# Kernel optimization log

Measured on AMD Instinct MI355X. Metric: run time of the kernel, lower is better.

Reference implementation:

```python
import jax, jax.numpy as jnp
import numpy as np

STRIDES = (8, 16, 32, 64, 128)
SIZES = ((40, 40), (20, 20), (10, 10), (5, 5), (3, 3))
NUM_CLASSES = 80
SCORE_THR = 0.025
NMS_PRE = 1000
IOU_THR = 0.5
IMG = 320.0  # img_shape hardcoded to (320, 320); clamp uses max_shape[1]
B = 4


def setup_inputs() -> dict:
    key = jax.random.key(0)
    ks = jax.random.split(key, 15)
    inp = {}
    for i, (h, w) in enumerate(SIZES):
        inp[f"cls{i}"] = jax.random.normal(ks[3 * i], (B, NUM_CLASSES, h, w), dtype=jnp.float32)
        # bbox preds are ltrb distances; scale uniform noise to plausible pixel distances
        inp[f"bbox{i}"] = jax.random.uniform(ks[3 * i + 1], (B, 4, h, w), dtype=jnp.float32) * 64.0
        inp[f"ctr{i}"] = jax.random.normal(ks[3 * i + 2], (B, 1, h, w), dtype=jnp.float32)
    return inp


def _priors(h, w, stride):
    # MlvlPointGenerator: (arange + 0.5) * stride, x fastest-varying
    sx = (jnp.arange(w, dtype=jnp.float32) + 0.5) * stride
    sy = (jnp.arange(h, dtype=jnp.float32) + 0.5) * stride
    return jnp.stack([jnp.tile(sx, h), jnp.repeat(sy, w)], axis=-1)  # [h*w, 2]


def _distance2bbox(points, dist):
    x1 = points[:, 0] - dist[:, 0]
    y1 = points[:, 1] - dist[:, 1]
    x2 = points[:, 0] + dist[:, 2]
    y2 = points[:, 1] + dist[:, 3]
    # torch.clamp_ on the whole tensor: min=0, max=max_shape[1]=320
    return jnp.clip(jnp.stack([x1, y1, x2, y2], axis=-1), 0.0, IMG)


def _pairwise_iou(boxes):
    # torchvision-style IoU on [K,4] boxes
    area = (boxes[:, 2] - boxes[:, 0]) * (boxes[:, 3] - boxes[:, 1])
    lt = jnp.maximum(boxes[:, None, :2], boxes[None, :, :2])
    rb = jnp.minimum(boxes[:, None, 2:], boxes[None, :, 2:])
    wh = jnp.maximum(rb - lt, 0.0)
    inter = wh[..., 0] * wh[..., 1]
    union = area[:, None] + area[None, :] - inter
    safe = jnp.where(union > 0.0, union, 1.0)
    return jnp.where(union > 0.0, inter / safe, 0.0)


def _single(cls_l, bbox_l, ctr_l):
    """Post-process one image. Returns fixed-size (dets [K,5], labels [K], keep [K] bool)."""
    scores_l, labels_l, boxes_l, valid_l = [], [], [], []
    for lvl in range(5):
        h, w = SIZES[lvl]
        pri = _priors(h, w, STRIDES[lvl])
        s = jax.nn.sigmoid(jnp.transpose(cls_l[lvl], (1, 2, 0)).reshape(-1, NUM_CLASSES)).reshape(-1)
        bp = jnp.transpose(bbox_l[lvl], (1, 2, 0)).reshape(-1, 4)
        sf = jax.nn.sigmoid(jnp.transpose(ctr_l[lvl], (1, 2, 0)).reshape(-1))
        # filter_scores_and_topk: mask scores <= thr to -1 so they sort last; fixed-size top_k
        k = min(NMS_PRE, s.shape[0])
        top_s, top_i = jax.lax.top_k(jnp.where(s > SCORE_THR, s, -1.0), k)
        anchor = top_i // NUM_CLASSES
        label = top_i % NUM_CLASSES
        valid = top_s > SCORE_THR
        boxes = _distance2bbox(pri[anchor], bp[anchor])
        # scores multiplied by centerness score factor (FCOS)
        scores_l.append(jnp.where(valid, top_s * sf[anchor], -1.0))
        labels_l.append(label)
        boxes_l.append(boxes)
        valid_l.append(valid)
    scores = jnp.concatenate(scores_l)          # [K]
    labels = jnp.concatenate(labels_l)          # [K]
    boxes = jnp.concatenate(boxes_l, axis=0)    # [K,4]
    valid = jnp.concatenate(valid_l)            # [K]
    # sort by final score descending (NMS processes in score order)
    order = jnp.argsort(-scores)
    scores = scores[order]
    labels = labels[order]
    boxes = boxes[order]
    valid = valid[order]
    # batched_nms: per-class coordinate offset trick
    max_coord = boxes.max()
    off = boxes + (labels.astype(jnp.float32) * (max_coord + 1.0))[:, None]
    iou = _pairwise_iou(off)  # [K,K]
    K = scores.shape[0]
    idx = jnp.arange(K)

    def body(i, keep):
        sup = (iou[i] > IOU_THR) & (idx > i) & keep[i]
        return keep & jnp.logical_not(sup)

    keep = jax.lax.fori_loop(0, K, body, valid)
    dets = jnp.concatenate([boxes, scores[:, None]], axis=-1)  # [K,5]
    return dets, labels, keep


def reference(cls0, cls1, cls2, cls3, cls4, bbox0, bbox1, bbox2, bbox3, bbox4, ctr0, ctr1, ctr2, ctr3, ctr4):
    cls_l = (cls0, cls1, cls2, cls3, cls4)
    bbox_l = (bbox0, bbox1, bbox2, bbox3, bbox4)
    ctr_l = (ctr0, ctr1, ctr2, ctr3, ctr4)
    return jax.vmap(_single)(cls_l, bbox_l, ctr_l)
```

## Files before the change

### kernel.cpp

```cpp
#include <hip/hip_runtime.h>
#include <stdint.h>


#define BN 4
#define NC 80
#define TOT 170720
#define KTOT 4720
#define NWIN 74
#define NJT 19
#define TIE_CAP 4096
#define IMGSZ 320.0f
#define PAIR_CAP 131072
#define LDSP 12288

struct InPtrs {
  const float* cls[5];
  const float* bbox[5];
  const float* ctr[5];
};

__device__ __forceinline__ uint32_t f2s(float f) {
  uint32_t x = __float_as_uint(f);
  return (x & 0x80000000u) ? ~x : (x | 0x80000000u);
}
__device__ __forceinline__ float s2f(uint32_t s) {
  uint32_t x = (s & 0x80000000u) ? (s & 0x7fffffffu) : ~s;
  return __uint_as_float(x);
}
__device__ __forceinline__ float sigmoid32(float v) {
  float e = (float)exp(-(double)v);
  return __fdiv_rn(1.0f, __fadd_rn(1.0f, e));
}
__device__ __forceinline__ void lvl_of(int e, int& l, int& le) {
  if (e < 128000)      { l = 0; le = e; }
  else if (e < 160000) { l = 1; le = e - 128000; }
  else if (e < 168000) { l = 2; le = e - 160000; }
  else if (e < 170000) { l = 3; le = e - 168000; }
  else                 { l = 4; le = e - 170000; }
}
__device__ __forceinline__ int kl_of(int l) {
  constexpr int KL[5] = {1000, 1000, 1000, 1000, 720};
  return KL[l];
}
__device__ __forceinline__ float clip32(float v) {
  return fminf(fmaxf(v, 0.0f), IMGSZ);
}
__device__ __forceinline__ void tile_of(int t, int& l, int& p0) {
  if (t < 25)       { l = 0; p0 = t * 64; }
  else if (t < 32)  { l = 1; p0 = (t - 25) * 64; }
  else if (t < 34)  { l = 2; p0 = (t - 32) * 64; }
  else if (t == 34) { l = 3; p0 = 0; }
  else              { l = 4; p0 = 0; }
}
__device__ __forceinline__ int iou_gt(float bx1, float by1, float bx2, float by2,
                                      float bai, float4 o) {
  float ta_ = __fmul_rn(__fsub_rn(o.z, o.x), __fsub_rn(o.w, o.y));
  float ltx = fmaxf(bx1, o.x), lty = fmaxf(by1, o.y);
  float rbx = fminf(bx2, o.z), rby = fminf(by2, o.w);
  float wd = fmaxf(__fsub_rn(rbx, ltx), 0.0f);
  float hg = fmaxf(__fsub_rn(rby, lty), 0.0f);
  float inter = __fmul_rn(wd, hg);
  float asum = __fadd_rn(bai, ta_);
  float uni  = __fsub_rn(asum, inter);
  float iou  = (uni > 0.0f) ? __fdiv_rn(inter, uni) : 0.0f;
  return (iou > 0.5f) ? 1 : 0;
}

__global__ void k_score(InPtrs in, uint32_t* __restrict__ su, uint32_t* __restrict__ hist0) {
  int b = blockIdx.y;
  int tl, p0; tile_of(blockIdx.x, tl, p0);
  constexpr int HWc[5]  = {1600, 400, 100, 25, 9};
  constexpr int LOFF[5] = {0, 128000, 160000, 168000, 170000};
  int hw = HWc[tl];
  int tw = min(64, hw - p0);
  int tid = threadIdx.x;
  __shared__ uint32_t lu[64 * 81];
  __shared__ uint32_t lh[1024];
  for (int i = tid; i < 1024; i += 256) lh[i] = 0;
  __syncthreads();
  int pf = tid & 63;
  if (pf < tw) {
    const float* cp = in.cls[tl] + (size_t)b * NC * hw + p0 + pf;
    for (int c = tid >> 6; c < NC; c += 4) {
      float v = cp[(size_t)c * hw];
      float s = sigmoid32(v);
      float m = (s > 0.025f) ? s : -1.0f;
      uint32_t u = f2s(m);
      lu[pf * 81 + c] = u;
      atomicAdd(&lh[u >> 22], 1u);
    }
  }
  __syncthreads();
  int bl = b * 5 + tl;
  for (int i = tid; i < 1024; i += 256)
    if (lh[i]) atomicAdd(&hist0[(size_t)bl * 1024 + i], lh[i]);
  int n = tw * NC;
  uint32_t* dst = su + (size_t)b * TOT + LOFF[tl] + p0 * NC;
  for (int idx = tid; idx < n; idx += 256)
    dst[idx] = lu[(idx / 80) * 81 + (idx % 80)];
}

__global__ void k_scan1(const uint32_t* __restrict__ su, const uint32_t* __restrict__ mpfx,
                        uint32_t* __restrict__ hist1) {
  int b = blockIdx.y;
  int tid = threadIdx.x;
  int e0 = blockIdx.x * 256;
  int e = e0 + tid;
  int l0, le0; lvl_of(e0, l0, le0);
  __shared__ uint32_t lh[2][1024];
  for (int i = tid; i < 2048; i += 256) lh[i >> 10][i & 1023] = 0;
  __syncthreads();
  if (e < TOT) {
    int l, le; lvl_of(e, l, le);
    uint32_t C = mpfx[b * 5 + l];
    uint32_t u = su[(size_t)b * TOT + e];
    if ((u >> 22) == (C >> 22)) atomicAdd(&lh[l - l0][(u >> 12) & 1023u], 1u);
  }
  __syncthreads();
  for (int s = 0; s < 2; s++) {
    int l = l0 + s;
    if (l >= 5) break;
    int bl = b * 5 + l;
    for (int i = tid; i < 1024; i += 256)
      if (lh[s][i]) atomicAdd(&hist1[(size_t)bl * 1024 + i], lh[s][i]);
  }
}

__global__ void k_scan2(const uint32_t* __restrict__ su, const uint32_t* __restrict__ mpfx,
                        uint32_t* __restrict__ hist2) {
  int b = blockIdx.y;
  int e = blockIdx.x * blockDim.x + threadIdx.x;
  if (e >= TOT) return;
  int l, le; lvl_of(e, l, le);
  int bl = b * 5 + l;
  uint32_t C = mpfx[bl];
  uint32_t u = su[(size_t)b * TOT + e];
  if ((u >> 12) == (C >> 12))
    atomicAdd(&hist2[(size_t)bl * 4096 + (u & 4095u)], 1u);
}

__global__ void k_findp(const uint32_t* __restrict__ hist, uint32_t* __restrict__ mpfx,
                        uint32_t* __restrict__ mk, int nbins, int shift, int pass) {
  int bl = blockIdx.x;
  uint32_t k = (pass == 0) ? (uint32_t)kl_of(bl % 5) : mk[bl];
  const uint32_t* h = hist + (size_t)bl * nbins;
  __shared__ uint32_t gsum[256];
  int tid = threadIdx.x;
  int per = nbins / 256;
  int base = tid * per;
  uint32_t s = 0;
  for (int i = 0; i < per; i++) s += h[base + i];
  gsum[tid] = s;
  __syncthreads();
  uint32_t above = 0;
  for (int t = tid + 1; t < 256; t++) above += gsum[t];
  if (above < k && above + s >= k) {
    uint32_t cum = above;
    for (int bin = base + per - 1; bin >= base; bin--) {
      uint32_t c = h[bin];
      if (cum < k && cum + c >= k) {
        uint32_t pfx = (pass == 0) ? 0u : mpfx[bl];
        mpfx[bl] = pfx | ((uint32_t)bin << shift);
        mk[bl] = k - cum;
        break;
      }
      cum += c;
    }
  }
}

__global__ void k_compact(const uint32_t* __restrict__ su, const uint32_t* __restrict__ mpfx,
                          uint32_t* __restrict__ selcnt, uint32_t* __restrict__ tiecnt,
                          uint32_t* __restrict__ selu, uint32_t* __restrict__ seli,
                          uint32_t* __restrict__ tiei) {
  int b = blockIdx.y;
  int tid = threadIdx.x;
  int e0 = blockIdx.x * 256;
  int e = e0 + tid;
  int l0, le0; lvl_of(e0, l0, le0);
  __shared__ uint32_t cnt[2], tcnt[2], gbase[2], tgbase[2];
  __shared__ uint32_t su_s[2][256], si_s[2][256];
  __shared__ uint32_t ti_s[2][256];
  if (tid < 2) { cnt[tid] = 0u; tcnt[tid] = 0u; }
  __syncthreads();
  if (e < TOT) {
    int l, le; lvl_of(e, l, le);
    int slot = l - l0;
    int bl = b * 5 + l;
    uint32_t u = su[(size_t)b * TOT + e];
    uint32_t C = mpfx[bl];
    if (u > C) {
      uint32_t p = atomicAdd(&cnt[slot], 1u);
      su_s[slot][p] = u;
      si_s[slot][p] = (uint32_t)le;
    } else if (u == C) {
      uint32_t p = atomicAdd(&tcnt[slot], 1u);
      ti_s[slot][p] = (uint32_t)le;
    }
  }
  __syncthreads();
  if (tid < 2) {
    int bl = b * 5 + l0 + tid;
    if (cnt[tid])  gbase[tid]  = atomicAdd(&selcnt[bl], cnt[tid]);
    if (tcnt[tid]) tgbase[tid] = atomicAdd(&tiecnt[bl], tcnt[tid]);
  }
  __syncthreads();
  for (int s = 0; s < 2; s++) {
    int bl = b * 5 + l0 + s;
    uint32_t n = cnt[s];
    for (uint32_t t = tid; t < n; t += 256) {
      uint32_t pos = gbase[s] + t;
      selu[(size_t)bl * 1024 + pos] = su_s[s][t];
      seli[(size_t)bl * 1024 + pos] = si_s[s][t];
    }
    uint32_t tn = tcnt[s];
    for (uint32_t t = tid; t < tn; t += 256) {
      uint32_t pos = tgbase[s] + t;
      if (pos < TIE_CAP) tiei[(size_t)bl * TIE_CAP + pos] = ti_s[s][t];
    }
  }
}

__global__ void k_ties(const uint32_t* __restrict__ mpfx, const uint32_t* __restrict__ mk,
                       const uint32_t* __restrict__ tiecnt, const uint32_t* __restrict__ tiei,
                       uint32_t* __restrict__ selu, uint32_t* __restrict__ seli) {
  int bl = blockIdx.x;
  int l = bl % 5;
  uint32_t C = mpfx[bl];
  uint32_t T = mk[bl];
  uint32_t G = (uint32_t)kl_of(l) - T;
  uint32_t Tc = tiecnt[bl];
  if (Tc > TIE_CAP) Tc = TIE_CAP;
  __shared__ uint32_t sh[TIE_CAP];
  for (uint32_t t = threadIdx.x; t < Tc; t += blockDim.x) sh[t] = tiei[(size_t)bl * TIE_CAP + t];
  __syncthreads();
  for (uint32_t t = threadIdx.x; t < Tc; t += blockDim.x) {
    uint32_t my = sh[t];
    uint32_t rank = 0;
    for (uint32_t q = 0; q < Tc; q++) rank += (sh[q] < my) ? 1u : 0u;
    if (rank < T) {
      selu[(size_t)bl * 1024 + G + rank] = C;
      seli[(size_t)bl * 1024 + G + rank] = my;
    }
  }
}

__global__ void k_emit(InPtrs in, const uint32_t* __restrict__ selu, const uint32_t* __restrict__ seli,
                       float* __restrict__ ccs, uint32_t* __restrict__ ccl,
                       uint32_t* __restrict__ ccv, float* __restrict__ ccb) {
  int bl = blockIdx.x;
  int chunk = blockIdx.y;
  int b = bl / 5, l = bl % 5;
  int k = kl_of(l);
  __shared__ uint64_t z[1024];
  int tid = threadIdx.x;
  for (int t = tid; t < 1024; t += 256) {
    if (t < k) {
      uint32_t u = selu[(size_t)bl * 1024 + t];
      uint32_t idx = seli[(size_t)bl * 1024 + t];
      z[t] = (((uint64_t)u) << 32) | (uint32_t)(~idx);
    } else z[t] = 0ull;
  }
  __syncthreads();
  int tg = chunk * 256 + tid;
  if (tg >= k) return;
  uint64_t zi = z[tg];
  uint32_t u = (uint32_t)(zi >> 32);
  uint32_t idx = ~(uint32_t)zi;
  int rank = 0;
  const uint4* z4 = (const uint4*)z;
  for (int j4 = 0; j4 < 512; j4++) {
    uint4 q = z4[j4];
    uint64_t za = (((uint64_t)q.y) << 32) | q.x;
    uint64_t zb = (((uint64_t)q.w) << 32) | q.z;
    rank += (za > zi) ? 1 : 0;
    rank += (zb > zi) ? 1 : 0;
  }
  constexpr int Wc[5]  = {40, 20, 10, 5, 3};
  constexpr int HWc[5] = {1600, 400, 100, 25, 9};
  constexpr float Sc[5] = {8.f, 16.f, 32.f, 64.f, 128.f};
  constexpr int COFF[5] = {0, 1000, 2000, 3000, 4000};
  int w = Wc[l], hw = HWc[l];
  float ms = s2f(u);
  int valid = (ms > 0.025f) ? 1 : 0;
  int p = (int)idx / NC, c = (int)idx % NC;
  int x = p % w, y = p / w;
  float sf = sigmoid32(in.ctr[l][(size_t)b * hw + p]);
  float score = valid ? __fmul_rn(ms, sf) : -1.0f;
  float px = __fmul_rn(__fadd_rn((float)x, 0.5f), Sc[l]);
  float py = __fmul_rn(__fadd_rn((float)y, 0.5f), Sc[l]);
  size_t bb = (size_t)b * 4 * hw;
  float d0 = in.bbox[l][bb + 0 * hw + p];
  float d1 = in.bbox[l][bb + 1 * hw + p];
  float d2 = in.bbox[l][bb + 2 * hw + p];
  float d3 = in.bbox[l][bb + 3 * hw + p];
  float x1 = clip32(__fsub_rn(px, d0)), y1 = clip32(__fsub_rn(py, d1));
  float x2 = clip32(__fadd_rn(px, d2)), y2 = clip32(__fadd_rn(py, d3));
  int o = b * KTOT + COFF[l] + rank;
  ccs[o] = score;
  ccl[o] = (uint32_t)c;
  ccv[o] = (uint32_t)valid;
  ccb[(size_t)o * 4 + 0] = x1; ccb[(size_t)o * 4 + 1] = y1;
  ccb[(size_t)o * 4 + 2] = x2; ccb[(size_t)o * 4 + 3] = y2;
}

__global__ void k_rank(const float* __restrict__ ccs, uint32_t* __restrict__ rankp) {
  int b = blockIdx.z;
  int jt = blockIdx.y;
  int ib = blockIdx.x;
  int tid = threadIdx.x;
  __shared__ uint32_t jk[256];
  int j0 = jt * 256;
  int jn = min(256, KTOT - j0);
  jk[tid] = (tid < jn) ? f2s(ccs[(size_t)b * KTOT + j0 + tid]) : 0u;
  __syncthreads();
  int e = ib * 256 + tid;
  if (e >= KTOT) return;
  uint32_t ke = f2s(ccs[(size_t)b * KTOT + e]);
  int rank = 0;
  const uint4* k4 = (const uint4*)jk;
#pragma unroll 8
  for (int q = 0; q < 64; q++) {
    uint4 kk = k4[q];
    int j = j0 + q * 4;
    rank += ((kk.x > ke) || (kk.x == ke && (j + 0) < e)) ? 1 : 0;
    rank += ((kk.y > ke) || (kk.y == ke && (j + 1) < e)) ? 1 : 0;
    rank += ((kk.z > ke) || (kk.z == ke && (j + 2) < e)) ? 1 : 0;
    rank += ((kk.w > ke) || (kk.w == ke && (j + 3) < e)) ? 1 : 0;
  }
  rankp[((size_t)b * NJT + jt) * KTOT + e] = (uint32_t)rank;
}

__global__ void k_scatter(const float* __restrict__ ccs, const uint32_t* __restrict__ ccl,
                          const uint32_t* __restrict__ ccv, const float* __restrict__ ccb,
                          const uint32_t* __restrict__ rankp,
                          float* __restrict__ ss, uint32_t* __restrict__ sl,
                          uint32_t* __restrict__ sv, float* __restrict__ sb,
                          uint32_t* __restrict__ maxcb) {
  int b = blockIdx.y;
  __shared__ float red[4];
  int tid = threadIdx.x;
  int e = blockIdx.x * 256 + tid;
  float mx = 0.0f;
  if (e < KTOT) {
    uint32_t rank = 0;
    for (int jt = 0; jt < NJT; jt++)
      rank += rankp[((size_t)b * NJT + jt) * KTOT + e];
    int sidx = b * KTOT + e;
    int d = b * KTOT + (int)rank;
    ss[d] = ccs[sidx];
    sl[d] = ccl[sidx];
    sv[d] = ccv[sidx];
    float b0 = ccb[(size_t)sidx * 4 + 0], b1 = ccb[(size_t)sidx * 4 + 1];
    float b2 = ccb[(size_t)sidx * 4 + 2], b3 = ccb[(size_t)sidx * 4 + 3];
    sb[(size_t)d * 4 + 0] = b0; sb[(size_t)d * 4 + 1] = b1;
    sb[(size_t)d * 4 + 2] = b2; sb[(size_t)d * 4 + 3] = b3;
    mx = fmaxf(fmaxf(b0, b1), fmaxf(b2, b3));
  }
  for (int o = 32; o; o >>= 1) mx = fmaxf(mx, __shfl_xor(mx, o));
  if ((tid & 63) == 0) red[tid >> 6] = mx;
  __syncthreads();
  if (tid == 0)
    atomicMax(&maxcb[b], __float_as_uint(fmaxf(fmaxf(red[0], red[1]), fmaxf(red[2], red[3]))));
}

__global__ void k_bits(const uint32_t* __restrict__ sv, unsigned long long* __restrict__ vbits) {
  int w = blockIdx.x, b = blockIdx.y, lane = threadIdx.x;
  int e = w * 64 + lane;
  int pred = (e < KTOT) ? (sv[(size_t)b * KTOT + e] != 0u) : 0;
  unsigned long long m = __ballot(pred);
  if (lane == 0) vbits[b * NWIN + w] = m;
}

__global__ void k_offset(const float* __restrict__ sb, const uint32_t* __restrict__ sl,
                         const uint32_t* __restrict__ maxcb, float* __restrict__ ob,
                         uint32_t* __restrict__ paircnt) {
  if (blockIdx.x == 0 && threadIdx.x < BN) paircnt[threadIdx.x] = 0u;
  int r = blockIdx.x * blockDim.x + threadIdx.x;
  if (r >= BN * KTOT) return;
  int b = r / KTOT;
  float scale = __fadd_rn(__uint_as_float(maxcb[b]), 1.0f);
  float offv = __fmul_rn((float)sl[r], scale);
  float x1 = __fadd_rn(sb[(size_t)r * 4 + 0], offv);
  float y1 = __fadd_rn(sb[(size_t)r * 4 + 1], offv);
  float x2 = __fadd_rn(sb[(size_t)r * 4 + 2], offv);
  float y2 = __fadd_rn(sb[(size_t)r * 4 + 3], offv);
  ob[(size_t)r * 4 + 0] = x1; ob[(size_t)r * 4 + 1] = y1;
  ob[(size_t)r * 4 + 2] = x2; ob[(size_t)r * 4 + 3] = y2;
}

__global__ void k_class(const uint32_t* __restrict__ sl, uint32_t* __restrict__ clist,
                        uint32_t* __restrict__ ccount) {
  int b = blockIdx.y;
  int c = blockIdx.x;
  int tid = threadIdx.x;
  int lane = tid & 63, wv = tid >> 6;
  __shared__ uint32_t woff[4];
  uint32_t* out = clist + ((size_t)b * NC + c) * KTOT;
  uint32_t base = 0;
  for (int chunk = 0; chunk < KTOT; chunk += 256) {
    int e = chunk + tid;
    int pred = (e < KTOT) && (sl[(size_t)b * KTOT + e] == (uint32_t)c);
    unsigned long long bal = __ballot(pred);
    if (lane == 0) woff[wv] = (uint32_t)__popcll(bal);
    __syncthreads();
    uint32_t myoff = base;
    for (int v = 0; v < wv; v++) myoff += woff[v];
    uint32_t tot = woff[0] + woff[1] + woff[2] + woff[3];
    if (pred) {
      uint32_t pos = myoff + (uint32_t)__popcll(bal & ((1ull << lane) - 1ull));
      out[pos] = (uint32_t)e;
    }
    base += tot;
    __syncthreads();
  }
  if (tid == 0) ccount[b * NC + c] = base;
}

__global__ void k_mask2(const float* __restrict__ ob, const uint32_t* __restrict__ clist,
                        const uint32_t* __restrict__ ccount,
                        uint32_t* __restrict__ pairs, uint32_t* __restrict__ paircnt) {
  int b = blockIdx.y;
  int c = blockIdx.x;
  int m = (int)ccount[b * NC + c];
  if (m < 2) return;
  const uint32_t* cl = clist + ((size_t)b * NC + c) * KTOT;
  const float4* ob4 = (const float4*)ob + (size_t)b * KTOT;
  int tid = threadIdx.x;
  __shared__ float4 tb[256];
  __shared__ uint32_t jidx[256];
  __shared__ uint32_t pcnt[256];
  __shared__ uint32_t sbase;
  uint32_t mycnt = 0;
  for (int jt = 0; jt < m; jt += 256) {
    int jn = min(256, m - jt);
    __syncthreads();
    if (tid < jn) { uint32_t gj = cl[jt + tid]; jidx[tid] = gj; tb[tid] = ob4[gj]; }
    __syncthreads();
    for (int i = tid; i < m; i += 256) {
      uint32_t gi = cl[i];
      float4 v = ob4[gi];
      float bai = __fmul_rn(__fsub_rn(v.z, v.x), __fsub_rn(v.w, v.y));
      for (int jj = 0; jj < jn; jj++)
        if (jidx[jj] > gi && iou_gt(v.x, v.y, v.z, v.w, bai, tb[jj])) mycnt++;
    }
  }
  __syncthreads();
  pcnt[tid] = mycnt;
  __syncthreads();
  uint32_t myoff = 0, total = 0;
  for (int t = 0; t < 256; t++) { uint32_t v = pcnt[t]; if (t < tid) myoff += v; total += v; }
  if (total == 0) return;
  if (tid == 0) sbase = atomicAdd(&paircnt[b], total);
  __syncthreads();
  uint32_t base = sbase;
  uint32_t* gp = pairs + (size_t)b * PAIR_CAP;
  uint32_t k = 0;
  for (int jt = 0; jt < m; jt += 256) {
    int jn = min(256, m - jt);
    __syncthreads();
    if (tid < jn) { uint32_t gj = cl[jt + tid]; jidx[tid] = gj; tb[tid] = ob4[gj]; }
    __syncthreads();
    for (int i = tid; i < m; i += 256) {
      uint32_t gi = cl[i];
      float4 v = ob4[gi];
      float bai = __fmul_rn(__fsub_rn(v.z, v.x), __fsub_rn(v.w, v.y));
      for (int jj = 0; jj < jn; jj++) {
        uint32_t gj = jidx[jj];
        if (gj > gi && iou_gt(v.x, v.y, v.z, v.w, bai, tb[jj])) {
          uint32_t pos = base + myoff + k; k++;
          if (pos < PAIR_CAP) gp[pos] = (gi << 13) | gj;
        }
      }
    }
  }
}

__global__ void k_nms(const float* __restrict__ ob,
                      const unsigned long long* __restrict__ vbits,
                      unsigned long long* __restrict__ keepw,
                      const uint32_t* __restrict__ pairs,
                      const uint32_t* __restrict__ paircnt) {
  int b = blockIdx.x;
  int tid = threadIdx.x;
  int lane = tid & 63;
  int wv = tid >> 6;
  __shared__ unsigned long long tdl[NWIN * 64];
  __shared__ unsigned long long svl[NWIN];
  __shared__ unsigned long long sup[NWIN];
  __shared__ unsigned long long kwsh;
  __shared__ uint32_t plp[LDSP];
  __shared__ uint32_t wstart[NWIN + 1];
  __shared__ uint32_t wtmp[NWIN];
  for (int i = tid; i < NWIN * 64; i += 256) tdl[i] = 0ull;
  if (tid < NWIN) { svl[tid] = vbits[b * NWIN + tid]; sup[tid] = 0ull; wtmp[tid] = 0u; }
  uint32_t npairs = paircnt[b];
  bool useP = (npairs <= (uint32_t)PAIR_CAP);
  bool useL = (npairs <= (uint32_t)LDSP);
  const uint32_t* gpl = pairs + (size_t)b * PAIR_CAP;
  __syncthreads();
  unsigned int* sup32 = (unsigned int*)sup;
  unsigned int* tdl32 = (unsigned int*)tdl;
  if (useP) {
    for (uint32_t t = tid; t < npairs; t += 256) {
      uint32_t p = gpl[t];
      int i = (int)(p >> 13), j = (int)(p & 8191u);
      if ((i >> 6) == (j >> 6)) {
        int r = ((i >> 6) * 64 + (i & 63)) * 2 + ((j & 63) >> 5);
        atomicOr(&tdl32[r], 1u << (j & 31));
      } else {
        atomicAdd(&wtmp[i >> 6], 1u);
      }
    }
    __syncthreads();
    if (tid == 0) {
      uint32_t acc = 0;
      for (int w = 0; w < NWIN; w++) { wstart[w] = acc; acc += wtmp[w]; }
      wstart[NWIN] = acc;
    }
    __syncthreads();
    if (tid < NWIN) wtmp[tid] = 0u;
    __syncthreads();
    if (useL) {
      for (uint32_t t = tid; t < npairs; t += 256) {
        uint32_t p = gpl[t];
        int i = (int)(p >> 13), j = (int)(p & 8191u);
        if ((i >> 6) == (j >> 6)) continue;
        uint32_t w = (uint32_t)(i >> 6);
        uint32_t pos = wstart[w] + atomicAdd(&wtmp[w], 1u);
        plp[pos] = p;
      }
    }
    __syncthreads();
    for (int w = 0; w < NWIN; w++) {
      if (wv == 0) {
        unsigned long long row = tdl[w * 64 + lane];
        unsigned long long m = __ballot(row != 0ull);
        unsigned long long sa = sup[w];
        unsigned long long sval = svl[w];
        unsigned int rlo = (unsigned int)row, rhi = (unsigned int)(row >> 32);
        while (m) {
          int i = __ffsll((long long)m) - 1;
          m &= m - 1;
          if (((sval >> i) & 1ull) && !((sa >> i) & 1ull)) {
            unsigned int lo = (unsigned int)__builtin_amdgcn_readlane((int)rlo, i);
            unsigned int hi = (unsigned int)__builtin_amdgcn_readlane((int)rhi, i);
            sa |= (((unsigned long long)hi) << 32) | (unsigned long long)lo;
          }
        }
        unsigned long long kw = sval & ~sa;
        if (lane == 0) { keepw[b * NWIN + w] = kw; kwsh = kw; }
      }
      __syncthreads();
      unsigned long long kw = kwsh;
      if (useL) {
        for (uint32_t t = wstart[w] + tid; t < wstart[w + 1]; t += 256) {
          uint32_t p = plp[t];
          int i = (int)(p >> 13);
          if (!((kw >> (i & 63)) & 1ull)) continue;
          int j = (int)(p & 8191u);
          atomicOr(&sup32[j >> 5], 1u << (j & 31));
        }
      } else {
        for (uint32_t t = tid; t < npairs; t += 256) {
          uint32_t p = gpl[t];
          int i = (int)(p >> 13);
          if ((i >> 6) != w) continue;
          int j = (int)(p & 8191u);
          if ((j >> 6) == w) continue;
          if (!((kw >> (i & 63)) & 1ull)) continue;
          atomicOr(&sup32[j >> 5], 1u << (j & 31));
        }
      }
      __syncthreads();
    }
  } else {
    const float4* ob4 = (const float4*)ob + (size_t)b * KTOT;
    for (int w = 0; w < NWIN; w++) {
      if (wv == 0) {
        int i = w * 64 + lane;
        unsigned long long row = 0ull;
        if (i < KTOT) {
          float4 v = ob4[i];
          float bai = __fmul_rn(__fsub_rn(v.z, v.x), __fsub_rn(v.w, v.y));
          for (int jj = 0; jj < 64; jj++) {
            int j = w * 64 + jj;
            if (j > i && j < KTOT)
              row |= ((unsigned long long)iou_gt(v.x, v.y, v.z, v.w, bai, ob4[j])) << jj;
          }
        }
        unsigned long long m = __ballot(row != 0ull);
        unsigned long long sa = sup[w];
        unsigned long long sval = svl[w];
        unsigned int rlo = (unsigned int)row, rhi = (unsigned int)(row >> 32);
        while (m) {
          int i2 = __ffsll((long long)m) - 1;
          m &= m - 1;
          if (((sval >> i2) & 1ull) && !((sa >> i2) & 1ull)) {
            unsigned int lo = (unsigned int)__builtin_amdgcn_readlane((int)rlo, i2);
            unsigned int hi = (unsigned int)__builtin_amdgcn_readlane((int)rhi, i2);
            sa |= (((unsigned long long)hi) << 32) | (unsigned long long)lo;
          }
        }
        unsigned long long kw = sval & ~sa;
        if (lane == 0) { keepw[b * NWIN + w] = kw; kwsh = kw; }
      }
      __syncthreads();
      unsigned long long kw = kwsh;
      for (int ii = 0; ii < 64; ii++) {
        if (!((kw >> ii) & 1ull)) continue;
        int i = w * 64 + ii;
        if (i >= KTOT) break;
        float4 v = ob4[i];
        float bai = __fmul_rn(__fsub_rn(v.z, v.x), __fsub_rn(v.w, v.y));
        for (int j = (w + 1) * 64 + tid; j < KTOT; j += 256)
          if (iou_gt(v.x, v.y, v.z, v.w, bai, ob4[j]))
            atomicOr(&sup32[j >> 5], 1u << (j & 31));
      }
      __syncthreads();
    }
  }
}

__global__ void k_out(const float* __restrict__ ss, const uint32_t* __restrict__ sl,
                      const float* __restrict__ sb, const unsigned long long* __restrict__ keepw,
                      float* __restrict__ out) {
  int r = blockIdx.x * blockDim.x + threadIdx.x;
  if (r >= BN * KTOT) return;
  int b = r / KTOT;
  int e = r - b * KTOT;
  unsigned int kp = (unsigned int)((keepw[b * NWIN + (e >> 6)] >> (e & 63)) & 1ull);
  out[(size_t)r * 5 + 0] = sb[(size_t)r * 4 + 0];
  out[(size_t)r * 5 + 1] = sb[(size_t)r * 4 + 1];
  out[(size_t)r * 5 + 2] = sb[(size_t)r * 4 + 2];
  out[(size_t)r * 5 + 3] = sb[(size_t)r * 4 + 3];
  out[(size_t)r * 5 + 4] = ss[r];
  out[(size_t)BN * KTOT * 5 + r] = (float)sl[r];
  out[(size_t)BN * KTOT * 6 + r] = kp ? 1.0f : 0.0f;
}

extern "C" void kernel_launch(void* const* d_in, const int* in_sizes, int n_in,
                              void* d_out, int out_size, void* d_ws, size_t ws_size,
                              hipStream_t stream) {
  InPtrs ip;
  for (int l = 0; l < 5; l++) {
    ip.cls[l]  = (const float*)d_in[3 * l + 0];
    ip.bbox[l] = (const float*)d_in[3 * l + 1];
    ip.ctr[l]  = (const float*)d_in[3 * l + 2];
  }

  size_t off = 0;
  auto alloc = [&](size_t n) {
    char* p = (char*)d_ws + off;
    off = (off + n + 255) & ~(size_t)255;
    return p;
  };
  const size_t SU_BYTES   = (size_t)BN * TOT * 4;
  const size_t HIST_BYTES = (20ull * 1024 + 20ull * 1024 + 20ull * 4096) * 4;
  const size_t EXTRA      = 256;
  char* r0p = (char*)alloc(((SU_BYTES + 255) & ~(size_t)255) + HIST_BYTES + EXTRA);
  uint32_t* su    = (uint32_t*)r0p;
  uint32_t* hist0 = (uint32_t*)(r0p + ((SU_BYTES + 255) & ~(size_t)255));
  uint32_t* hist1 = hist0 + 20ull * 1024;
  uint32_t* hist2 = hist1 + 20ull * 1024;
  uint32_t* selcnt = hist2 + 20ull * 4096;
  uint32_t* tiecnt = selcnt + 20;
  uint32_t* maxcb  = tiecnt + 20;

  uint32_t* mpfx   = (uint32_t*)alloc(20 * 4);
  uint32_t* mk     = (uint32_t*)alloc(20 * 4);
  uint32_t* selu   = (uint32_t*)alloc(20ull * 1024 * 4);
  uint32_t* seli   = (uint32_t*)alloc(20ull * 1024 * 4);
  uint32_t* tiei   = (uint32_t*)alloc(20ull * TIE_CAP * 4);
  float*    ccs    = (float*)   alloc((size_t)BN * KTOT * 4);
  uint32_t* ccl    = (uint32_t*)alloc((size_t)BN * KTOT * 4);
  uint32_t* ccv    = (uint32_t*)alloc((size_t)BN * KTOT * 4);
  float*    ccb    = (float*)   alloc((size_t)BN * KTOT * 16);
  float*    ss     = (float*)   alloc((size_t)BN * KTOT * 4);
  uint32_t* sl     = (uint32_t*)alloc((size_t)BN * KTOT * 4);
  uint32_t* sv     = (uint32_t*)alloc((size_t)BN * KTOT * 4);
  float*    sb     = (float*)   alloc((size_t)BN * KTOT * 16);
  float*    ob     = (float*)   alloc((size_t)BN * KTOT * 16);
  uint32_t* rankp  = (uint32_t*)alloc((size_t)BN * NJT * KTOT * 4);
  uint32_t* clist  = (uint32_t*)alloc((size_t)BN * NC * KTOT * 4);
  uint32_t* ccount = (uint32_t*)alloc((size_t)BN * NC * 4);
  unsigned long long* vbits = (unsigned long long*)alloc((size_t)BN * NWIN * 8);
  unsigned long long* keepw = (unsigned long long*)alloc((size_t)BN * NWIN * 8);
  uint32_t* pairs   = (uint32_t*)alloc((size_t)BN * PAIR_CAP * 4);
  uint32_t* paircnt = (uint32_t*)alloc(BN * 4);
  (void)ws_size; (void)in_sizes; (void)n_in; (void)out_size;

  dim3 gscan((TOT + 255) / 256, BN);
  hipMemsetAsync(hist0, 0, HIST_BYTES + EXTRA, stream);
  k_score<<<dim3(36, BN), 256, 0, stream>>>(ip, su, hist0);
  k_findp<<<20, 256, 0, stream>>>(hist0, mpfx, mk, 1024, 22, 0);
  k_scan1<<<gscan, 256, 0, stream>>>(su, mpfx, hist1);
  k_findp<<<20, 256, 0, stream>>>(hist1, mpfx, mk, 1024, 12, 1);
  k_scan2<<<gscan, 256, 0, stream>>>(su, mpfx, hist2);
  k_findp<<<20, 256, 0, stream>>>(hist2, mpfx, mk, 4096, 0, 2);
  k_compact<<<gscan, 256, 0, stream>>>(su, mpfx, selcnt, tiecnt, selu, seli, tiei);
  k_ties<<<20, 256, 0, stream>>>(mpfx, mk, tiecnt, tiei, selu, seli);
  k_emit<<<dim3(20, 4), 256, 0, stream>>>(ip, selu, seli, ccs, ccl, ccv, ccb);
  k_rank<<<dim3(19, NJT, BN), 256, 0, stream>>>(ccs, rankp);
  k_scatter<<<dim3(19, BN), 256, 0, stream>>>(ccs, ccl, ccv, ccb, rankp, ss, sl, sv, sb, maxcb);
  k_class<<<dim3(NC, BN), 256, 0, stream>>>(sl, clist, ccount);
  k_bits<<<dim3(NWIN, BN), 64, 0, stream>>>(sv, vbits);
  k_offset<<<(BN * KTOT + 255) / 256, 256, 0, stream>>>(sb, sl, maxcb, ob, paircnt);
  k_mask2<<<dim3(NC, BN), 256, 0, stream>>>(ob, clist, ccount, pairs, paircnt);
  k_nms<<<BN, 256, 0, stream>>>(ob, vbits, keepw, pairs, paircnt);
  k_out<<<(BN * KTOT + 255) / 256, 256, 0, stream>>>(ss, sl, sb, keepw, (float*)d_out);
}
```

Baseline: 267.7 us.

## Fuse offset/bits and class-list/pair kernels; run NMS window loop in one wave

Merges k_offset and k_bits into one kernel, and k_class and k_mask2 into one kernel that keeps the per-class index list in LDS instead of a global clist buffer. In k_nms, the per-window suppression propagation now runs entirely in the first wavefront, replacing two block-wide barriers per window with a block-level fence. This cuts two launches, global round-trips and 148 __syncthreads, but pair propagation now uses 64 lanes instead of 256, and the fused pair kernel uses about 19KB more LDS.

```diff
diff --git a/kernel.cpp b/kernel.cpp
--- a/kernel.cpp
+++ b/kernel.cpp
@@ -364,39 +364,44 @@
     atomicMax(&maxcb[b], __float_as_uint(fmaxf(fmaxf(red[0], red[1]), fmaxf(red[2], red[3]))));
 }
 
-__global__ void k_bits(const uint32_t* __restrict__ sv, unsigned long long* __restrict__ vbits) {
-  int w = blockIdx.x, b = blockIdx.y, lane = threadIdx.x;
-  int e = w * 64 + lane;
-  int pred = (e < KTOT) ? (sv[(size_t)b * KTOT + e] != 0u) : 0;
+__global__ void k_offbits(const float* __restrict__ sb, const uint32_t* __restrict__ sl,
+                          const uint32_t* __restrict__ maxcb, const uint32_t* __restrict__ sv,
+                          float* __restrict__ ob, unsigned long long* __restrict__ vbits,
+                          uint32_t* __restrict__ paircnt) {
+  int b = blockIdx.y;
+  int tid = threadIdx.x;
+  if (blockIdx.x == 0 && b == 0 && tid < BN) paircnt[tid] = 0u;
+  int e = blockIdx.x * 256 + tid;
+  int pred = 0;
+  if (e < KTOT) {
+    int r = b * KTOT + e;
+    float scale = __fadd_rn(__uint_as_float(maxcb[b]), 1.0f);
+    float offv = __fmul_rn((float)sl[r], scale);
+    float x1 = __fadd_rn(sb[(size_t)r * 4 + 0], offv);
+    float y1 = __fadd_rn(sb[(size_t)r * 4 + 1], offv);
+    float x2 = __fadd_rn(sb[(size_t)r * 4 + 2], offv);
+    float y2 = __fadd_rn(sb[(size_t)r * 4 + 3], offv);
+    ob[(size_t)r * 4 + 0] = x1; ob[(size_t)r * 4 + 1] = y1;
+    ob[(size_t)r * 4 + 2] = x2; ob[(size_t)r * 4 + 3] = y2;
+    pred = (sv[r] != 0u);
+  }
   unsigned long long m = __ballot(pred);
-  if (lane == 0) vbits[b * NWIN + w] = m;
-}
-
-__global__ void k_offset(const float* __restrict__ sb, const uint32_t* __restrict__ sl,
-                         const uint32_t* __restrict__ maxcb, float* __restrict__ ob,
-                         uint32_t* __restrict__ paircnt) {
-  if (blockIdx.x == 0 && threadIdx.x < BN) paircnt[threadIdx.x] = 0u;
-  int r = blockIdx.x * blockDim.x + threadIdx.x;
-  if (r >= BN * KTOT) return;
-  int b = r / KTOT;
-  float scale = __fadd_rn(__uint_as_float(maxcb[b]), 1.0f);
-  float offv = __fmul_rn((float)sl[r], scale);
-  float x1 = __fadd_rn(sb[(size_t)r * 4 + 0], offv);
-  float y1 = __fadd_rn(sb[(size_t)r * 4 + 1], offv);
-  float x2 = __fadd_rn(sb[(size_t)r * 4 + 2], offv);
-  float y2 = __fadd_rn(sb[(size_t)r * 4 + 3], offv);
-  ob[(size_t)r * 4 + 0] = x1; ob[(size_t)r * 4 + 1] = y1;
-  ob[(size_t)r * 4 + 2] = x2; ob[(size_t)r * 4 + 3] = y2;
-}
-
-__global__ void k_class(const uint32_t* __restrict__ sl, uint32_t* __restrict__ clist,
-                        uint32_t* __restrict__ ccount) {
+  int w = blockIdx.x * 4 + (tid >> 6);
+  if ((tid & 63) == 0 && w < NWIN) vbits[b * NWIN + w] = m;
+}
+
+__global__ void k_pairs(const uint32_t* __restrict__ sl, const float* __restrict__ ob,
+                        uint32_t* __restrict__ pairs, uint32_t* __restrict__ paircnt) {
   int b = blockIdx.y;
   int c = blockIdx.x;
   int tid = threadIdx.x;
   int lane = tid & 63, wv = tid >> 6;
+  __shared__ uint32_t lst[KTOT];
   __shared__ uint32_t woff[4];
-  uint32_t* out = clist + ((size_t)b * NC + c) * KTOT;
+  __shared__ float4 tb[256];
+  __shared__ uint32_t jidx[256];
+  __shared__ uint32_t pcnt[256];
+  __shared__ uint32_t sbase;
   uint32_t base = 0;
   for (int chunk = 0; chunk < KTOT; chunk += 256) {
     int e = chunk + tid;
@@ -407,38 +412,21 @@
     uint32_t myoff = base;
     for (int v = 0; v < wv; v++) myoff += woff[v];
     uint32_t tot = woff[0] + woff[1] + woff[2] + woff[3];
-    if (pred) {
-      uint32_t pos = myoff + (uint32_t)__popcll(bal & ((1ull << lane) - 1ull));
-      out[pos] = (uint32_t)e;
-    }
+    if (pred) lst[myoff + (uint32_t)__popcll(bal & ((1ull << lane) - 1ull))] = (uint32_t)e;
     base += tot;
     __syncthreads();
   }
-  if (tid == 0) ccount[b * NC + c] = base;
-}
-
-__global__ void k_mask2(const float* __restrict__ ob, const uint32_t* __restrict__ clist,
-                        const uint32_t* __restrict__ ccount,
-                        uint32_t* __restrict__ pairs, uint32_t* __restrict__ paircnt) {
-  int b = blockIdx.y;
-  int c = blockIdx.x;
-  int m = (int)ccount[b * NC + c];
+  int m = (int)base;
   if (m < 2) return;
-  const uint32_t* cl = clist + ((size_t)b * NC + c) * KTOT;
   const float4* ob4 = (const float4*)ob + (size_t)b * KTOT;
-  int tid = threadIdx.x;
-  __shared__ float4 tb[256];
-  __shared__ uint32_t jidx[256];
-  __shared__ uint32_t pcnt[256];
-  __shared__ uint32_t sbase;
   uint32_t mycnt = 0;
   for (int jt = 0; jt < m; jt += 256) {
     int jn = min(256, m - jt);
     __syncthreads();
-    if (tid < jn) { uint32_t gj = cl[jt + tid]; jidx[tid] = gj; tb[tid] = ob4[gj]; }
+    if (tid < jn) { uint32_t gj = lst[jt + tid]; jidx[tid] = gj; tb[tid] = ob4[gj]; }
     __syncthreads();
     for (int i = tid; i < m; i += 256) {
-      uint32_t gi = cl[i];
+      uint32_t gi = lst[i];
       float4 v = ob4[gi];
       float bai = __fmul_rn(__fsub_rn(v.z, v.x), __fsub_rn(v.w, v.y));
       for (int jj = 0; jj < jn; jj++)
@@ -453,22 +441,22 @@
   if (total == 0) return;
   if (tid == 0) sbase = atomicAdd(&paircnt[b], total);
   __syncthreads();
-  uint32_t base = sbase;
+  uint32_t gb = sbase;
   uint32_t* gp = pairs + (size_t)b * PAIR_CAP;
   uint32_t k = 0;
   for (int jt = 0; jt < m; jt += 256) {
     int jn = min(256, m - jt);
     __syncthreads();
-    if (tid < jn) { uint32_t gj = cl[jt + tid]; jidx[tid] = gj; tb[tid] = ob4[gj]; }
+    if (tid < jn) { uint32_t gj = lst[jt + tid]; jidx[tid] = gj; tb[tid] = ob4[gj]; }
     __syncthreads();
     for (int i = tid; i < m; i += 256) {
-      uint32_t gi = cl[i];
+      uint32_t gi = lst[i];
       float4 v = ob4[gi];
       float bai = __fmul_rn(__fsub_rn(v.z, v.x), __fsub_rn(v.w, v.y));
       for (int jj = 0; jj < jn; jj++) {
         uint32_t gj = jidx[jj];
         if (gj > gi && iou_gt(v.x, v.y, v.z, v.w, bai, tb[jj])) {
-          uint32_t pos = base + myoff + k; k++;
+          uint32_t pos = gb + myoff + k; k++;
           if (pos < PAIR_CAP) gp[pos] = (gi << 13) | gj;
         }
       }
@@ -484,7 +472,6 @@
   int b = blockIdx.x;
   int tid = threadIdx.x;
   int lane = tid & 63;
-  int wv = tid >> 6;
   __shared__ unsigned long long tdl[NWIN * 64];
   __shared__ unsigned long long svl[NWIN];
   __shared__ unsigned long long sup[NWIN];
@@ -532,8 +519,8 @@
       }
     }
     __syncthreads();
-    for (int w = 0; w < NWIN; w++) {
-      if (wv == 0) {
+    if (tid < 64) {
+      for (int w = 0; w < NWIN; w++) {
         unsigned long long row = tdl[w * 64 + lane];
         unsigned long long m = __ballot(row != 0ull);
         unsigned long long sa = sup[w];
@@ -549,32 +536,31 @@
           }
         }
         unsigned long long kw = sval & ~sa;
-        if (lane == 0) { keepw[b * NWIN + w] = kw; kwsh = kw; }
+        if (lane == 0) keepw[b * NWIN + w] = kw;
+        if (useL) {
+          for (uint32_t t = wstart[w] + lane; t < wstart[w + 1]; t += 64) {
+            uint32_t p = plp[t];
+            int i = (int)(p >> 13);
+            if (!((kw >> (i & 63)) & 1ull)) continue;
+            int j = (int)(p & 8191u);
+            atomicOr(&sup32[j >> 5], 1u << (j & 31));
+          }
+        } else {
+          for (uint32_t t = lane; t < npairs; t += 64) {
+            uint32_t p = gpl[t];
+            int i = (int)(p >> 13);
+            if ((i >> 6) != w) continue;
+            int j = (int)(p & 8191u);
+            if ((j >> 6) == w) continue;
+            if (!((kw >> (i & 63)) & 1ull)) continue;
+            atomicOr(&sup32[j >> 5], 1u << (j & 31));
+          }
+        }
+        __threadfence_block();
       }
-      __syncthreads();
-      unsigned long long kw = kwsh;
-      if (useL) {
-        for (uint32_t t = wstart[w] + tid; t < wstart[w + 1]; t += 256) {
-          uint32_t p = plp[t];
-          int i = (int)(p >> 13);
-          if (!((kw >> (i & 63)) & 1ull)) continue;
-          int j = (int)(p & 8191u);
-          atomicOr(&sup32[j >> 5], 1u << (j & 31));
-        }
-      } else {
-        for (uint32_t t = tid; t < npairs; t += 256) {
-          uint32_t p = gpl[t];
-          int i = (int)(p >> 13);
-          if ((i >> 6) != w) continue;
-          int j = (int)(p & 8191u);
-          if ((j >> 6) == w) continue;
-          if (!((kw >> (i & 63)) & 1ull)) continue;
-          atomicOr(&sup32[j >> 5], 1u << (j & 31));
-        }
-      }
-      __syncthreads();
     }
   } else {
+    int wv = tid >> 6;
     const float4* ob4 = (const float4*)ob + (size_t)b * KTOT;
     for (int w = 0; w < NWIN; w++) {
       if (wv == 0) {
@@ -682,8 +668,6 @@
   float*    sb     = (float*)   alloc((size_t)BN * KTOT * 16);
   float*    ob     = (float*)   alloc((size_t)BN * KTOT * 16);
   uint32_t* rankp  = (uint32_t*)alloc((size_t)BN * NJT * KTOT * 4);
-  uint32_t* clist  = (uint32_t*)alloc((size_t)BN * NC * KTOT * 4);
-  uint32_t* ccount = (uint32_t*)alloc((size_t)BN * NC * 4);
   unsigned long long* vbits = (unsigned long long*)alloc((size_t)BN * NWIN * 8);
   unsigned long long* keepw = (unsigned long long*)alloc((size_t)BN * NWIN * 8);
   uint32_t* pairs   = (uint32_t*)alloc((size_t)BN * PAIR_CAP * 4);
@@ -703,10 +687,8 @@
   k_emit<<<dim3(20, 4), 256, 0, stream>>>(ip, selu, seli, ccs, ccl, ccv, ccb);
   k_rank<<<dim3(19, NJT, BN), 256, 0, stream>>>(ccs, rankp);
   k_scatter<<<dim3(19, BN), 256, 0, stream>>>(ccs, ccl, ccv, ccb, rankp, ss, sl, sv, sb, maxcb);
-  k_class<<<dim3(NC, BN), 256, 0, stream>>>(sl, clist, ccount);
-  k_bits<<<dim3(NWIN, BN), 64, 0, stream>>>(sv, vbits);
-  k_offset<<<(BN * KTOT + 255) / 256, 256, 0, stream>>>(sb, sl, maxcb, ob, paircnt);
-  k_mask2<<<dim3(NC, BN), 256, 0, stream>>>(ob, clist, ccount, pairs, paircnt);
+  k_offbits<<<dim3(19, BN), 256, 0, stream>>>(sb, sl, maxcb, sv, ob, vbits, paircnt);
+  k_pairs<<<dim3(NC, BN), 256, 0, stream>>>(sl, ob, pairs, paircnt);
   k_nms<<<BN, 256, 0, stream>>>(ob, vbits, keepw, pairs, paircnt);
   k_out<<<(BN * KTOT + 255) / 256, 256, 0, stream>>>(ss, sl, sb, keepw, (float*)d_out);
 }
```

New measurement: 260.0 us. -2.9%, faster.
